# Kernel optimization log

Measured on AMD Instinct MI355X. Metric: run time of the kernel, lower is better.

Reference implementation:

```python
import jax, jax.numpy as jnp
import numpy as np

B, SQ, SK, D, H, DH = 4, 1024, 1024, 1024, 16, 64  # transform_units*head_units == 1024


def setup_inputs() -> dict:
    key = jax.random.key(0)
    ks = jax.random.split(key, 8)
    q = jax.random.normal(ks[0], (B, SQ, D), dtype=jnp.float32)
    v = jax.random.normal(ks[1], (B, SK, D), dtype=jnp.float32)
    q_mask = jax.random.randint(ks[2], (B, SQ), 0, 2).astype(bool).at[:, 0].set(True)
    v_mask = jax.random.randint(ks[3], (B, SK), 0, 2).astype(bool).at[:, 0].set(True)
    s = 0.02
    Wq = jax.random.normal(ks[4], (D, H * DH), dtype=jnp.float32) * s
    Wk = jax.random.normal(ks[5], (D, H * DH), dtype=jnp.float32) * s
    Wv = jax.random.normal(ks[6], (D, H * DH), dtype=jnp.float32) * s
    Wo = jax.random.normal(ks[7], (H * DH, D), dtype=jnp.float32) * s
    bq = jnp.zeros((H * DH,), jnp.float32)
    bk = jnp.zeros((H * DH,), jnp.float32)
    bv = jnp.zeros((H * DH,), jnp.float32)
    bo = jnp.zeros((D,), jnp.float32)
    return {"q": q, "v": v, "q_mask": q_mask, "v_mask": v_mask,
            "Wq": Wq, "bq": bq, "Wk": Wk, "bk": bk, "Wv": Wv, "bv": bv,
            "Wo": Wo, "bo": bo}


def reference(q, v, q_mask, v_mask, Wq, bq, Wk, bk, Wv, bv, Wo, bo):
    # k = v in the original module
    k = v
    # QKV projections; split-last-dim + batch-concat trick == reshape to heads
    Q = (q @ Wq + bq).reshape(B, SQ, H, DH)
    Kh = (k @ Wk + bk).reshape(B, SK, H, DH)
    V = (v @ Wv + bv).reshape(B, SK, H, DH)
    # Keras Attention: unscaled dot-product scores
    scores = jnp.einsum('bqhd,bkhd->bhqk', Q, Kh)  # [B,H,SQ,SK]
    scores = jnp.where(v_mask[:, None, None, :], scores, jnp.float32(-1e9))
    attn = jax.nn.softmax(scores, axis=-1)
    ctx = jnp.einsum('bhqk,bkhd->bqhd', attn, V).reshape(B, SQ, H * DH)
    # Keras Attention zeros masked query positions before output dense
    ctx = ctx * q_mask[:, :, None].astype(ctx.dtype)
    return ctx @ Wo + bo
```

## Files before the change

kernel.cpp:

```cpp
#include <hip/hip_runtime.h>
#include <hip/hip_fp16.h>

typedef __attribute__((ext_vector_type(8))) _Float16 f16x8;
typedef __attribute__((ext_vector_type(4))) float f32x4;

__device__ __forceinline__ void gload_lds16(const _Float16* g, _Float16* l) {
  __builtin_amdgcn_global_load_lds((const __attribute__((address_space(1))) void*)g,
                                   (__attribute__((address_space(3))) void*)l, 16, 0, 0);
}

__global__ __launch_bounds__(256) void prep_kernel(
    const float* __restrict__ q, const float* __restrict__ v,
    const float* __restrict__ W0, const float* __restrict__ W1,
    const float* __restrict__ W2, const float* __restrict__ W3,
    _Float16* __restrict__ q16, _Float16* __restrict__ v16,
    _Float16* __restrict__ T0, _Float16* __restrict__ T1,
    _Float16* __restrict__ T2, _Float16* __restrict__ T3) {
  __shared__ float tile[64 * 65];
  int tid = threadIdx.x, ybl = blockIdx.y;
  if (ybl < 16) {
    int i = (ybl * 256 + blockIdx.x) * 256 + tid;
    float4 fq = ((const float4*)q)[i];
    float4 fv = ((const float4*)v)[i];
    union { _Float16 h[4]; uint2 u; } oq, ov;
    oq.h[0] = (_Float16)fq.x; oq.h[1] = (_Float16)fq.y;
    oq.h[2] = (_Float16)fq.z; oq.h[3] = (_Float16)fq.w;
    ov.h[0] = (_Float16)fv.x; ov.h[1] = (_Float16)fv.y;
    ov.h[2] = (_Float16)fv.z; ov.h[3] = (_Float16)fv.w;
    *(uint2*)&q16[4 * (size_t)i] = oq.u;
    *(uint2*)&v16[4 * (size_t)i] = ov.u;
    return;
  }
  int z = ybl - 16;
  const float* W = (z == 0) ? W0 : (z == 1) ? W1 : (z == 2) ? W2 : W3;
  _Float16* T = (z == 0) ? T0 : (z == 1) ? T1 : (z == 2) ? T2 : T3;
  int bx = (blockIdx.x & 15) * 64, by = (blockIdx.x >> 4) * 64;
  for (int it = 0; it < 4; it++) {
    int lin = it * 256 + tid;
    int r = lin >> 4, q4 = (lin & 15) * 4;
    float4 f = *(const float4*)&W[(size_t)(by + r) * 1024 + bx + q4];
    tile[r * 65 + q4 + 0] = f.x;
    tile[r * 65 + q4 + 1] = f.y;
    tile[r * 65 + q4 + 2] = f.z;
    tile[r * 65 + q4 + 3] = f.w;
  }
  __syncthreads();
  for (int it = 0; it < 2; it++) {
    int lin = it * 256 + tid;
    int orow = lin >> 3, seg = (lin & 7) * 8;
    union { uint4 u; _Float16 h[8]; } o;
    for (int e = 0; e < 8; e++) o.h[e] = (_Float16)tile[(seg + e) * 65 + orow];
    *(uint4*)&T[(size_t)(bx + orow) * 1024 + by + seg] = o.u;
  }
}

__global__ __launch_bounds__(256) void gemm_qkv_kernel(
    const _Float16* __restrict__ q16, const _Float16* __restrict__ v16,
    const _Float16* __restrict__ WqT, const _Float16* __restrict__ WkT,
    const _Float16* __restrict__ WvT,
    const float* __restrict__ bq, const float* __restrict__ bk, const float* __restrict__ bv,
    _Float16* __restrict__ Q16, _Float16* __restrict__ K16, _Float16* __restrict__ VT16) {
  int z = blockIdx.z;
  const _Float16* A = (z == 0) ? q16 : v16;
  const _Float16* BT = (z == 0) ? WqT : ((z == 1) ? WkT : WvT);
  const float* bias = (z == 0) ? bq : ((z == 1) ? bk : bv);
  int m0 = blockIdx.y * 128, n0 = blockIdx.x * 128;
  const int K = 1024;

  __shared__ _Float16 Alds[2][128 * 64];
  __shared__ _Float16 Blds[2][128 * 64];
  int tid = threadIdx.x, lane = tid & 63, w = tid >> 6;
  int c = lane & 15, g = lane >> 4;
  int wm = (w & 1) * 64, wn = (w >> 1) * 64;
  int lr = lane >> 3;
  int ls = ((lane & 7) ^ lr) * 8;

  const _Float16* ga[4]; const _Float16* gb[4];
  int loff[4];
  for (int p = 0; p < 4; p++) {
    int chunk = w * 4 + p;
    int row = chunk * 8 + lr;
    ga[p] = &A[(size_t)(m0 + row) * K + ls];
    gb[p] = &BT[(size_t)(n0 + row) * K + ls];
    loff[p] = chunk * 512;
  }

  f32x4 acc[4][4];
  for (int i = 0; i < 4; i++)
    for (int j = 0; j < 4; j++)
      acc[i][j] = (f32x4){0.f, 0.f, 0.f, 0.f};

  for (int p = 0; p < 4; p++) {
    gload_lds16(ga[p], &Alds[0][loff[p]]);
    gload_lds16(gb[p], &Blds[0][loff[p]]);
  }
  __syncthreads();

  int xa = (c & 7) << 4;
  int cur = 0;
  for (int kt = 0; kt < 16; kt++) {
    if (kt + 1 < 16) {
      int nb = cur ^ 1;
      for (int p = 0; p < 4; p++) {
        gload_lds16(ga[p] + (kt + 1) * 64, &Alds[nb][loff[p]]);
        gload_lds16(gb[p] + (kt + 1) * 64, &Blds[nb][loff[p]]);
      }
    }
    const char* ab = (const char*)&Alds[cur][0];
    const char* bb = (const char*)&Blds[cur][0];
    for (int ks = 0; ks < 2; ks++) {
      f16x8 af[4], bf[4];
      for (int i = 0; i < 4; i++)
        af[i] = *(const f16x8*)(ab + (wm + i * 16 + c) * 128 + ((ks * 64 + g * 16) ^ xa));
      for (int j = 0; j < 4; j++)
        bf[j] = *(const f16x8*)(bb + (wn + j * 16 + c) * 128 + ((ks * 64 + g * 16) ^ xa));
      for (int i = 0; i < 4; i++)
        for (int j = 0; j < 4; j++)
          acc[i][j] = __builtin_amdgcn_mfma_f32_16x16x32_f16(af[i], bf[j], acc[i][j], 0, 0, 0);
    }
    __syncthreads();
    cur ^= 1;
  }

  if (z < 2) {
    _Float16* C = (z == 0) ? Q16 : K16;
    for (int j = 0; j < 4; j++) {
      float bv_ = bias[n0 + wn + j * 16 + c];
      for (int i = 0; i < 4; i++) {
        int r = m0 + wm + i * 16 + g * 4;
        int cc = n0 + wn + j * 16 + c;
        for (int e = 0; e < 4; e++)
          C[(size_t)(r + e) * 1024 + cc] = (_Float16)(acc[i][j][e] + bv_);
      }
    }
  } else {
    for (int j = 0; j < 4; j++) {
      int cc = n0 + wn + j * 16 + c;
      float bv_ = bias[cc];
      int h_ = cc >> 6, dh = cc & 63;
      for (int i = 0; i < 4; i++) {
        int r = m0 + wm + i * 16 + g * 4;
        int b_ = r >> 10, key = r & 1023;
        union { uint2 u; _Float16 hh[4]; } o;
        for (int e = 0; e < 4; e++) o.hh[e] = (_Float16)(acc[i][j][e] + bv_);
        *(uint2*)&VT16[((size_t)((b_ * 16 + h_) * 64 + dh)) * 1024 + key] = o.u;
      }
    }
  }
}

__global__ __launch_bounds__(256) void gemm_out_kernel(
    const _Float16* __restrict__ ctx16, const _Float16* __restrict__ WoT,
    const float* __restrict__ bo, float* __restrict__ out) {
  int m0 = blockIdx.y * 128, n0 = blockIdx.x * 64;
  const int K = 1024;
  __shared__ _Float16 Alds[2][128 * 64];
  __shared__ _Float16 Blds[2][64 * 64];
  int tid = threadIdx.x, lane = tid & 63, w = tid >> 6;
  int c = lane & 15, g = lane >> 4;
  int wm = (w & 1) * 64, wn = (w >> 1) * 32;
  int lr = lane >> 3;
  int ls = ((lane & 7) ^ lr) * 8;

  const _Float16* ga[4]; int laoff[4];
  const _Float16* gb[2]; int lboff[2];
  for (int p = 0; p < 4; p++) {
    int chunk = w * 4 + p;
    int row = chunk * 8 + lr;
    ga[p] = &ctx16[(size_t)(m0 + row) * K + ls];
    laoff[p] = chunk * 512;
  }
  for (int p = 0; p < 2; p++) {
    int chunk = w * 2 + p;
    int row = chunk * 8 + lr;
    gb[p] = &WoT[(size_t)(n0 + row) * K + ls];
    lboff[p] = chunk * 512;
  }

  f32x4 acc[4][2];
  for (int i = 0; i < 4; i++)
    for (int j = 0; j < 2; j++)
      acc[i][j] = (f32x4){0.f, 0.f, 0.f, 0.f};

  for (int p = 0; p < 4; p++) gload_lds16(ga[p], &Alds[0][laoff[p]]);
  for (int p = 0; p < 2; p++) gload_lds16(gb[p], &Blds[0][lboff[p]]);
  __syncthreads();

  int xa = (c & 7) << 4;
  int cur = 0;
  for (int kt = 0; kt < 16; kt++) {
    if (kt + 1 < 16) {
      int nb = cur ^ 1;
      for (int p = 0; p < 4; p++) gload_lds16(ga[p] + (kt + 1) * 64, &Alds[nb][laoff[p]]);
      for (int p = 0; p < 2; p++) gload_lds16(gb[p] + (kt + 1) * 64, &Blds[nb][lboff[p]]);
    }
    const char* ab = (const char*)&Alds[cur][0];
    const char* bb = (const char*)&Blds[cur][0];
    for (int ks = 0; ks < 2; ks++) {
      f16x8 af[4], bf[2];
      for (int i = 0; i < 4; i++)
        af[i] = *(const f16x8*)(ab + (wm + i * 16 + c) * 128 + ((ks * 64 + g * 16) ^ xa));
      for (int j = 0; j < 2; j++)
        bf[j] = *(const f16x8*)(bb + (wn + j * 16 + c) * 128 + ((ks * 64 + g * 16) ^ xa));
      for (int i = 0; i < 4; i++)
        for (int j = 0; j < 2; j++)
          acc[i][j] = __builtin_amdgcn_mfma_f32_16x16x32_f16(af[i], bf[j], acc[i][j], 0, 0, 0);
    }
    __syncthreads();
    cur ^= 1;
  }
  for (int j = 0; j < 2; j++) {
    float bv_ = bo[n0 + wn + j * 16 + c];
    for (int i = 0; i < 4; i++) {
      int r = m0 + wm + i * 16 + g * 4;
      int cc = n0 + wn + j * 16 + c;
      for (int e = 0; e < 4; e++)
        out[(size_t)(r + e) * 1024 + cc] = acc[i][j][e] + bv_;
    }
  }
}

__global__ __launch_bounds__(256, 4) void attn_kernel(
    const _Float16* __restrict__ Q16, const _Float16* __restrict__ K16,
    const _Float16* __restrict__ VT16,
    const int* __restrict__ q_mask, const int* __restrict__ v_mask,
    _Float16* __restrict__ ctx16) {
  int qb = blockIdx.x, h = blockIdx.y, b = blockIdx.z;
  int tid = threadIdx.x, lane = tid & 63, w = tid >> 6;
  int c = lane & 15, g = lane >> 4;
  int lr = lane >> 3, ls = lane & 7;

  __shared__ _Float16 QP[64 * 64];
  __shared__ _Float16 Kl[2][64 * 64];
  __shared__ _Float16 Vl[2][64 * 64];

  const _Float16* Qg = Q16 + ((size_t)(b * 1024 + qb * 64)) * 1024 + h * 64;
  const _Float16* Kg = K16 + ((size_t)(b * 1024)) * 1024 + h * 64;
  const _Float16* Vg = VT16 + ((size_t)(b * 16 + h)) * 64 * 1024;

  int row0 = w * 16 + lr, row1 = row0 + 8;
  int kx = (ls ^ lr) * 8;
  int ch0 = w * 2, ch1 = w * 2 + 1;

  gload_lds16(Qg + (size_t)row0 * 1024 + kx, QP + ch0 * 512);
  gload_lds16(Qg + (size_t)row1 * 1024 + kx, QP + ch1 * 512);
  gload_lds16(Kg + (size_t)row0 * 1024 + kx, &Kl[0][ch0 * 512]);
  gload_lds16(Kg + (size_t)row1 * 1024 + kx, &Kl[0][ch1 * 512]);
  gload_lds16(Vg + (size_t)row0 * 1024 + kx, &Vl[0][ch0 * 512]);
  gload_lds16(Vg + (size_t)row1 * 1024 + kx, &Vl[0][ch1 * 512]);
  __syncthreads();

  f16x8 qf[2];
  {
    int row = w * 16 + c;
    const char* rb = (const char*)QP + row * 128;
    int x = (row & 7) << 4;
    qf[0] = *(const f16x8*)(rb + ((g * 16) ^ x));
    qf[1] = *(const f16x8*)(rb + ((64 + g * 16) ^ x));
    const _Float16 l2e = (_Float16)1.44269504f;
    for (int e = 0; e < 8; e++) { qf[0][e] *= l2e; qf[1][e] *= l2e; }
  }

  float lp[4] = {0.f, 0.f, 0.f, 0.f};
  f32x4 acc_o[4];
  for (int jd = 0; jd < 4; jd++) acc_o[jd] = (f32x4){0.f, 0.f, 0.f, 0.f};

  char* pb = (char*)QP;
  int cur = 0;
  const float REF = -23.0831222f;
  for (int kb = 0; kb < 16; kb++) {
    if (kb + 1 < 16) {
      int nb = cur ^ 1;
      const _Float16* kgs = Kg + (size_t)(kb + 1) * 64 * 1024;
      const _Float16* vgs = Vg + (kb + 1) * 64;
      gload_lds16(kgs + (size_t)row0 * 1024 + kx, &Kl[nb][ch0 * 512]);
      gload_lds16(kgs + (size_t)row1 * 1024 + kx, &Kl[nb][ch1 * 512]);
      gload_lds16(vgs + (size_t)row0 * 1024 + kx, &Vl[nb][ch0 * 512]);
      gload_lds16(vgs + (size_t)row1 * 1024 + kx, &Vl[nb][ch1 * 512]);
    }
    float madd[4];
    for (int j = 0; j < 4; j++)
      madd[j] = v_mask[b * 1024 + kb * 64 + j * 16 + c] ? REF : -1e30f;

    f32x4 s[4];
    const char* kbse = (const char*)&Kl[cur][0];
    for (int j = 0; j < 4; j++) {
      int row = j * 16 + c;
      const char* rb = kbse + row * 128;
      int x = (row & 7) << 4;
      f16x8 k0 = *(const f16x8*)(rb + ((g * 16) ^ x));
      f16x8 k1 = *(const f16x8*)(rb + ((64 + g * 16) ^ x));
      s[j] = (f32x4){0.f, 0.f, 0.f, 0.f};
      s[j] = __builtin_amdgcn_mfma_f32_16x16x32_f16(qf[0], k0, s[j], 0, 0, 0);
      s[j] = __builtin_amdgcn_mfma_f32_16x16x32_f16(qf[1], k1, s[j], 0, 0, 0);
    }

    for (int j = 0; j < 4; j++)
      for (int e = 0; e < 4; e++) {
        float p = exp2f(s[j][e] + madd[j]);
        s[j][e] = p;
        lp[e] += p;
      }

    for (int j = 0; j < 4; j++)
      for (int e = 0; e < 4; e++) {
        int prow = w * 16 + g * 4 + e;
        int pby = prow * 128 + (((j * 16 + c) * 2) ^ ((prow & 7) << 4));
        *(_Float16*)(pb + pby) = (_Float16)s[j][e];
      }
    asm volatile("s_waitcnt lgkmcnt(0)" ::: "memory");
    __builtin_amdgcn_sched_barrier(0);

    const char* vbse = (const char*)&Vl[cur][0];
    for (int ks = 0; ks < 2; ks++) {
      int prow = w * 16 + c;
      f16x8 pf = *(const f16x8*)(pb + prow * 128 +
                                 ((ks * 64 + g * 16) ^ ((prow & 7) << 4)));
      for (int jd = 0; jd < 4; jd++) {
        int vrow = jd * 16 + c;
        f16x8 vf = *(const f16x8*)(vbse + vrow * 128 +
                                   ((ks * 64 + g * 16) ^ ((vrow & 7) << 4)));
        acc_o[jd] = __builtin_amdgcn_mfma_f32_16x16x32_f16(pf, vf, acc_o[jd], 0, 0, 0);
      }
    }

    __syncthreads();
    cur ^= 1;
  }

  for (int e = 0; e < 4; e++) {
    lp[e] += __shfl_xor(lp[e], 1);
    lp[e] += __shfl_xor(lp[e], 2);
    lp[e] += __shfl_xor(lp[e], 4);
    lp[e] += __shfl_xor(lp[e], 8);
  }

  int qrow = b * 1024 + qb * 64 + w * 16 + g * 4;
  float inv[4];
  for (int e = 0; e < 4; e++) {
    float qm = q_mask[qrow + e] ? 1.0f : 0.0f;
    inv[e] = qm / lp[e];
  }
  _Float16* cb = ctx16 + ((size_t)qrow) * 1024 + h * 64;
  for (int jd = 0; jd < 4; jd++)
    for (int e = 0; e < 4; e++)
      cb[(size_t)e * 1024 + jd * 16 + c] = (_Float16)(acc_o[jd][e] * inv[e]);
}

extern "C" void kernel_launch(void* const* d_in, const int* in_sizes, int n_in,
                              void* d_out, int out_size, void* d_ws, size_t ws_size,
                              hipStream_t stream) {
  const float* q  = (const float*)d_in[0];
  const float* v  = (const float*)d_in[1];
  const int* q_mask = (const int*)d_in[2];
  const int* v_mask = (const int*)d_in[3];
  const float* Wq = (const float*)d_in[4];
  const float* bq = (const float*)d_in[5];
  const float* Wk = (const float*)d_in[6];
  const float* bk = (const float*)d_in[7];
  const float* Wv = (const float*)d_in[8];
  const float* bv = (const float*)d_in[9];
  const float* Wo = (const float*)d_in[10];
  const float* bo = (const float*)d_in[11];
  float* out = (float*)d_out;

  _Float16* ws = (_Float16*)d_ws;
  const size_t NE = (size_t)4 * 1024 * 1024;
  _Float16* q16   = ws;
  _Float16* v16   = ws + NE;
  _Float16* Q16   = ws + 2 * NE;
  _Float16* K16   = ws + 3 * NE;
  _Float16* VT16  = ws + 4 * NE;
  _Float16* ctx16 = ws + 5 * NE;
  _Float16* WqT   = ws + 6 * NE;
  _Float16* WkT   = WqT + 1024 * 1024;
  _Float16* WvT   = WkT + 1024 * 1024;
  _Float16* WoT   = WvT + 1024 * 1024;

  prep_kernel<<<dim3(256, 20), 256, 0, stream>>>(q, v, Wq, Wk, Wv, Wo,
                                                 q16, v16, WqT, WkT, WvT, WoT);
  gemm_qkv_kernel<<<dim3(8, 32, 3), 256, 0, stream>>>(q16, v16, WqT, WkT, WvT,
                                                      bq, bk, bv, Q16, K16, VT16);
  attn_kernel<<<dim3(16, 16, 4), 256, 0, stream>>>(Q16, K16, VT16, q_mask, v_mask, ctx16);
  gemm_out_kernel<<<dim3(16, 32), 256, 0, stream>>>(ctx16, WoT, bo, out);
}
```

Before: 221.9 us.

## Halve GEMM K-tile to 32, add XCD-aware block remapping and occupancy hints

After: 201.7 us. 9.1% less time.

```diff
diff --git a/kernel.cpp b/kernel.cpp
--- a/kernel.cpp
+++ b/kernel.cpp
@@ -54,35 +54,37 @@
   }
 }
 
-__global__ __launch_bounds__(256) void gemm_qkv_kernel(
+__global__ __launch_bounds__(256, 3) void gemm_qkv_kernel(
     const _Float16* __restrict__ q16, const _Float16* __restrict__ v16,
     const _Float16* __restrict__ WqT, const _Float16* __restrict__ WkT,
     const _Float16* __restrict__ WvT,
     const float* __restrict__ bq, const float* __restrict__ bk, const float* __restrict__ bv,
     _Float16* __restrict__ Q16, _Float16* __restrict__ K16, _Float16* __restrict__ VT16) {
-  int z = blockIdx.z;
+  int ord = blockIdx.x + (blockIdx.y << 3) + (blockIdx.z << 8);
+  int wgid = (ord & 7) * 96 + (ord >> 3);
+  int z = wgid >> 8;
+  int rem = wgid & 255;
+  int m0 = (rem >> 3) * 128, n0 = (rem & 7) * 128;
+
   const _Float16* A = (z == 0) ? q16 : v16;
   const _Float16* BT = (z == 0) ? WqT : ((z == 1) ? WkT : WvT);
   const float* bias = (z == 0) ? bq : ((z == 1) ? bk : bv);
-  int m0 = blockIdx.y * 128, n0 = blockIdx.x * 128;
   const int K = 1024;
 
-  __shared__ _Float16 Alds[2][128 * 64];
-  __shared__ _Float16 Blds[2][128 * 64];
+  __shared__ _Float16 Alds[2][128 * 32];
+  __shared__ _Float16 Blds[2][128 * 32];
   int tid = threadIdx.x, lane = tid & 63, w = tid >> 6;
   int c = lane & 15, g = lane >> 4;
   int wm = (w & 1) * 64, wn = (w >> 1) * 64;
-  int lr = lane >> 3;
-  int ls = ((lane & 7) ^ lr) * 8;
-
-  const _Float16* ga[4]; const _Float16* gb[4];
-  int loff[4];
-  for (int p = 0; p < 4; p++) {
-    int chunk = w * 4 + p;
-    int row = chunk * 8 + lr;
-    ga[p] = &A[(size_t)(m0 + row) * K + ls];
-    gb[p] = &BT[(size_t)(n0 + row) * K + ls];
-    loff[p] = chunk * 512;
+  int rr = lane >> 2;
+  int su = ((lane & 3) ^ (rr & 3)) * 8;
+
+  const _Float16* gA[2]; const _Float16* gB[2]; int lo[2];
+  for (int p = 0; p < 2; p++) {
+    int row = w * 32 + p * 16 + rr;
+    gA[p] = &A[(size_t)(m0 + row) * K + su];
+    gB[p] = &BT[(size_t)(n0 + row) * K + su];
+    lo[p] = (w * 32 + p * 16) * 32;
   }
 
   f32x4 acc[4][4];
@@ -90,34 +92,32 @@
     for (int j = 0; j < 4; j++)
       acc[i][j] = (f32x4){0.f, 0.f, 0.f, 0.f};
 
-  for (int p = 0; p < 4; p++) {
-    gload_lds16(ga[p], &Alds[0][loff[p]]);
-    gload_lds16(gb[p], &Blds[0][loff[p]]);
+  for (int p = 0; p < 2; p++) {
+    gload_lds16(gA[p], &Alds[0][lo[p]]);
+    gload_lds16(gB[p], &Blds[0][lo[p]]);
   }
   __syncthreads();
 
-  int xa = (c & 7) << 4;
+  int xa = (c & 3) << 4;
   int cur = 0;
-  for (int kt = 0; kt < 16; kt++) {
-    if (kt + 1 < 16) {
+  for (int kt = 0; kt < 32; kt++) {
+    if (kt + 1 < 32) {
       int nb = cur ^ 1;
-      for (int p = 0; p < 4; p++) {
-        gload_lds16(ga[p] + (kt + 1) * 64, &Alds[nb][loff[p]]);
-        gload_lds16(gb[p] + (kt + 1) * 64, &Blds[nb][loff[p]]);
+      for (int p = 0; p < 2; p++) {
+        gload_lds16(gA[p] + (kt + 1) * 32, &Alds[nb][lo[p]]);
+        gload_lds16(gB[p] + (kt + 1) * 32, &Blds[nb][lo[p]]);
       }
     }
     const char* ab = (const char*)&Alds[cur][0];
     const char* bb = (const char*)&Blds[cur][0];
-    for (int ks = 0; ks < 2; ks++) {
-      f16x8 af[4], bf[4];
-      for (int i = 0; i < 4; i++)
-        af[i] = *(const f16x8*)(ab + (wm + i * 16 + c) * 128 + ((ks * 64 + g * 16) ^ xa));
+    f16x8 af[4], bf[4];
+    for (int i = 0; i < 4; i++)
+      af[i] = *(const f16x8*)(ab + (wm + i * 16 + c) * 64 + ((g * 16) ^ xa));
+    for (int j = 0; j < 4; j++)
+      bf[j] = *(const f16x8*)(bb + (wn + j * 16 + c) * 64 + ((g * 16) ^ xa));
+    for (int i = 0; i < 4; i++)
       for (int j = 0; j < 4; j++)
-        bf[j] = *(const f16x8*)(bb + (wn + j * 16 + c) * 128 + ((ks * 64 + g * 16) ^ xa));
-      for (int i = 0; i < 4; i++)
-        for (int j = 0; j < 4; j++)
-          acc[i][j] = __builtin_amdgcn_mfma_f32_16x16x32_f16(af[i], bf[j], acc[i][j], 0, 0, 0);
-    }
+        acc[i][j] = __builtin_amdgcn_mfma_f32_16x16x32_f16(af[i], bf[j], acc[i][j], 0, 0, 0);
     __syncthreads();
     cur ^= 1;
   }
@@ -149,32 +149,32 @@
   }
 }
 
-__global__ __launch_bounds__(256) void gemm_out_kernel(
+__global__ __launch_bounds__(256, 2) void gemm_out_kernel(
     const _Float16* __restrict__ ctx16, const _Float16* __restrict__ WoT,
     const float* __restrict__ bo, float* __restrict__ out) {
-  int m0 = blockIdx.y * 128, n0 = blockIdx.x * 64;
+  int ord = blockIdx.x + (blockIdx.y << 4);
+  int wgid = (ord & 7) * 64 + (ord >> 3);
+  int n0 = (wgid & 15) * 64, m0 = (wgid >> 4) * 128;
   const int K = 1024;
-  __shared__ _Float16 Alds[2][128 * 64];
-  __shared__ _Float16 Blds[2][64 * 64];
+  __shared__ _Float16 Alds[2][128 * 32];
+  __shared__ _Float16 Blds[2][64 * 32];
   int tid = threadIdx.x, lane = tid & 63, w = tid >> 6;
   int c = lane & 15, g = lane >> 4;
   int wm = (w & 1) * 64, wn = (w >> 1) * 32;
-  int lr = lane >> 3;
-  int ls = ((lane & 7) ^ lr) * 8;
-
-  const _Float16* ga[4]; int laoff[4];
-  const _Float16* gb[2]; int lboff[2];
-  for (int p = 0; p < 4; p++) {
-    int chunk = w * 4 + p;
-    int row = chunk * 8 + lr;
-    ga[p] = &ctx16[(size_t)(m0 + row) * K + ls];
-    laoff[p] = chunk * 512;
-  }
+  int rr = lane >> 2;
+  int su = ((lane & 3) ^ (rr & 3)) * 8;
+
+  const _Float16* gA[2]; int laoff[2];
   for (int p = 0; p < 2; p++) {
-    int chunk = w * 2 + p;
-    int row = chunk * 8 + lr;
-    gb[p] = &WoT[(size_t)(n0 + row) * K + ls];
-    lboff[p] = chunk * 512;
+    int row = w * 32 + p * 16 + rr;
+    gA[p] = &ctx16[(size_t)(m0 + row) * K + su];
+    laoff[p] = (w * 32 + p * 16) * 32;
+  }
+  const _Float16* gB; int lboff;
+  {
+    int row = w * 16 + rr;
+    gB = &WoT[(size_t)(n0 + row) * K + su];
+    lboff = (w * 16) * 32;
   }
 
   f32x4 acc[4][2];
@@ -182,30 +182,28 @@
     for (int j = 0; j < 2; j++)
       acc[i][j] = (f32x4){0.f, 0.f, 0.f, 0.f};
 
-  for (int p = 0; p < 4; p++) gload_lds16(ga[p], &Alds[0][laoff[p]]);
-  for (int p = 0; p < 2; p++) gload_lds16(gb[p], &Blds[0][lboff[p]]);
+  for (int p = 0; p < 2; p++) gload_lds16(gA[p], &Alds[0][laoff[p]]);
+  gload_lds16(gB, &Blds[0][lboff]);
   __syncthreads();
 
-  int xa = (c & 7) << 4;
+  int xa = (c & 3) << 4;
   int cur = 0;
-  for (int kt = 0; kt < 16; kt++) {
-    if (kt + 1 < 16) {
+  for (int kt = 0; kt < 32; kt++) {
+    if (kt + 1 < 32) {
       int nb = cur ^ 1;
-      for (int p = 0; p < 4; p++) gload_lds16(ga[p] + (kt + 1) * 64, &Alds[nb][laoff[p]]);
-      for (int p = 0; p < 2; p++) gload_lds16(gb[p] + (kt + 1) * 64, &Blds[nb][lboff[p]]);
+      for (int p = 0; p < 2; p++) gload_lds16(gA[p] + (kt + 1) * 32, &Alds[nb][laoff[p]]);
+      gload_lds16(gB + (kt + 1) * 32, &Blds[nb][lboff]);
     }
     const char* ab = (const char*)&Alds[cur][0];
     const char* bb = (const char*)&Blds[cur][0];
-    for (int ks = 0; ks < 2; ks++) {
-      f16x8 af[4], bf[2];
-      for (int i = 0; i < 4; i++)
-        af[i] = *(const f16x8*)(ab + (wm + i * 16 + c) * 128 + ((ks * 64 + g * 16) ^ xa));
+    f16x8 af[4], bf[2];
+    for (int i = 0; i < 4; i++)
+      af[i] = *(const f16x8*)(ab + (wm + i * 16 + c) * 64 + ((g * 16) ^ xa));
+    for (int j = 0; j < 2; j++)
+      bf[j] = *(const f16x8*)(bb + (wn + j * 16 + c) * 64 + ((g * 16) ^ xa));
+    for (int i = 0; i < 4; i++)
       for (int j = 0; j < 2; j++)
-        bf[j] = *(const f16x8*)(bb + (wn + j * 16 + c) * 128 + ((ks * 64 + g * 16) ^ xa));
-      for (int i = 0; i < 4; i++)
-        for (int j = 0; j < 2; j++)
-          acc[i][j] = __builtin_amdgcn_mfma_f32_16x16x32_f16(af[i], bf[j], acc[i][j], 0, 0, 0);
-    }
+        acc[i][j] = __builtin_amdgcn_mfma_f32_16x16x32_f16(af[i], bf[j], acc[i][j], 0, 0, 0);
     __syncthreads();
     cur ^= 1;
   }
@@ -225,7 +223,9 @@
     const _Float16* __restrict__ VT16,
     const int* __restrict__ q_mask, const int* __restrict__ v_mask,
     _Float16* __restrict__ ctx16) {
-  int qb = blockIdx.x, h = blockIdx.y, b = blockIdx.z;
+  int ord = blockIdx.x + (blockIdx.y << 4) + (blockIdx.z << 8);
+  int wgid = (ord & 7) * 128 + (ord >> 3);
+  int qb = wgid & 15, h = (wgid >> 4) & 15, b = wgid >> 8;
   int tid = threadIdx.x, lane = tid & 63, w = tid >> 6;
   int c = lane & 15, g = lane >> 4;
   int lr = lane >> 3, ls = lane & 7;
```
